# Optimization experiments

Measured on AMD Instinct MI355X. Metric: run time of the kernel, lower is better.

Reference implementation:

```python
import jax, jax.numpy as jnp
import numpy as np

B, N, E = 128, 196, 2048   # batch, num_features (14x14), encoder_dim
D, A = 512, 512            # decoder_dim, attention_dim


def setup_inputs() -> dict:
    key = jax.random.key(0)
    ks = jax.random.split(key, 8)
    s_e = 1.0 / np.sqrt(E)
    s_d = 1.0 / np.sqrt(D)
    s_a = 1.0 / np.sqrt(A)
    return {
        "encoder_out": jax.random.normal(ks[0], (B, N, E), dtype=jnp.float32),
        "decoder_hidden": jax.random.normal(ks[1], (B, D), dtype=jnp.float32),
        "We": jax.random.uniform(ks[2], (E, A), jnp.float32, -s_e, s_e),
        "be": jax.random.uniform(ks[3], (A,), jnp.float32, -s_e, s_e),
        "Wd": jax.random.uniform(ks[4], (D, A), jnp.float32, -s_d, s_d),
        "bd": jax.random.uniform(ks[5], (A,), jnp.float32, -s_d, s_d),
        "Wf": jax.random.uniform(ks[6], (A, 1), jnp.float32, -s_a, s_a),
        "bf": jax.random.uniform(ks[7], (1,), jnp.float32, -s_a, s_a),
    }


def reference(encoder_out, decoder_hidden, We, be, Wd, bd, Wf, bf):
    # att1: [B,N,A] projection of encoder features
    att1 = jnp.einsum('bne,ea->bna', encoder_out, We) + be
    # att2: [B,A] projection of decoder state, broadcast over N
    att2 = decoder_hidden @ Wd + bd
    att = jnp.tanh(att1 + att2[:, None, :])          # [B,N,A]
    scores = jnp.einsum('bna,ao->bno', att, Wf) + bf  # [B,N,1]
    alpha = jax.nn.softmax(scores, axis=1)            # softmax over num_features
    context = jnp.sum(encoder_out * alpha, axis=1)    # [B,E]
    return (context, alpha)
```

## Files before the change

### kernel.cpp

```cpp
#include <hip/hip_runtime.h>
#include <hip/hip_bf16.h>
#include <stdint.h>

#define B_   128
#define N_   196
#define E_   2048
#define D_   512
#define A_   512
#define MTOT (B_ * N_)

typedef short  short8  __attribute__((ext_vector_type(8)));
typedef float  floatx4 __attribute__((ext_vector_type(4)));

__device__ __forceinline__ unsigned short f2bf(float f) {
    union { float f; uint32_t u; } v; v.f = f;
    uint32_t r = v.u + 0x7FFFu + ((v.u >> 16) & 1u);
    return (unsigned short)(r >> 16);
}

__device__ __forceinline__ uint32_t pkbf(float a, float b) {
    uint32_t ua = __float_as_uint(a) + 0x8000u;
    uint32_t ub = __float_as_uint(b) + 0x8000u;
    return __builtin_amdgcn_perm(ub, ua, 0x07060302u);
}

__global__ void transcvt_k(const float* __restrict__ We, unsigned short* __restrict__ WeT) {
    __shared__ float tile[32][33];
    const int e0 = blockIdx.x * 32, a0 = blockIdx.y * 32;
    const int t = threadIdx.x, tc = t & 31, tr = t >> 5;
#pragma unroll
    for (int i = 0; i < 4; ++i) {
        int r = tr + i * 8;
        tile[r][tc] = We[(size_t)(e0 + r) * A_ + a0 + tc];
    }
    __syncthreads();
#pragma unroll
    for (int i = 0; i < 4; ++i) {
        int r = tr + i * 8;
        WeT[(size_t)(a0 + r) * E_ + e0 + tc] = f2bf(tile[tc][r]);
    }
}

__launch_bounds__(512)
__global__ void att2_k(const float* __restrict__ dh, const float* __restrict__ Wd,
                       const float* __restrict__ bd, const float* __restrict__ be,
                       float* __restrict__ att2p) {
    const int b = blockIdx.x, t = threadIdx.x;
    __shared__ float sdh[D_];
    sdh[t] = dh[b * D_ + t];
    __syncthreads();
    float acc = 0.f;
#pragma unroll 8
    for (int d = 0; d < D_; ++d) acc += sdh[d] * Wd[(size_t)d * A_ + t];
    att2p[(size_t)b * A_ + t] = acc + bd[t] + be[t];
}

__launch_bounds__(256, 4)
__global__ void score_gemm(const float* __restrict__ enc,
                           const unsigned short* __restrict__ WeT,
                           const float* __restrict__ att2p,
                           const float* __restrict__ Wf,
                           float* __restrict__ scoresP) {
    __shared__ __align__(16) char sMem[2 * 16384];
    __shared__ float sPart[2][128];

    const int t   = threadIdx.x;
    const int w   = t >> 6;
    const int l   = t & 63;
    const int l15 = l & 15;
    const int q4  = l >> 4;
    const int wr  = w >> 1, wc = w & 1;

    const int v     = (blockIdx.x & 7) * 98 + (blockIdx.x >> 3);
    const int strip = v >> 2, colb = v & 3;
    const int row0  = strip * 128;
    const int c0    = colb * 128;

    floatx4 acc[4][4] = {};

    const int ar = t >> 1, ah = t & 1;
    const float* aSrcT = enc + (size_t)(row0 + ar) * E_ + ah * 16;
    const int aswz = (ar >> 1) & 3;
    const int aWr0 = ar * 64 + (((2 * ah)     ^ aswz) * 16);
    const int aWr1 = ar * 64 + (((2 * ah + 1) ^ aswz) * 16);

    const unsigned short* bSrc[2];
    int bDst[2];
#pragma unroll
    for (int j = 0; j < 2; ++j) {
        int s = w * 2 + j;
        int n = s * 16 + (l >> 2), p = l & 3;
        int q = p ^ ((n >> 1) & 3);
        bSrc[j] = WeT + (size_t)(c0 + n) * E_ + q * 8;
        bDst[j] = 8192 + s * 1024;
    }

    const int chR  = q4 ^ ((l15 >> 1) & 3);
    const int offA = (wr * 64 + l15) * 64 + chR * 16;
    const int offB = 8192 + (wc * 64 + l15) * 64 + chR * 16;

    {
        float4 a0 = *(const float4*)(aSrcT);
        float4 a1 = *(const float4*)(aSrcT + 4);
        float4 a2 = *(const float4*)(aSrcT + 8);
        float4 a3 = *(const float4*)(aSrcT + 12);
#pragma unroll
        for (int j = 0; j < 2; ++j)
            __builtin_amdgcn_global_load_lds(
                (const __attribute__((address_space(1))) uint32_t*)(bSrc[j]),
                (__attribute__((address_space(3))) uint32_t*)(sMem + bDst[j]), 16, 0, 0);
        uint4 w0, w1;
        w0.x = pkbf(a0.x, a0.y); w0.y = pkbf(a0.z, a0.w);
        w0.z = pkbf(a1.x, a1.y); w0.w = pkbf(a1.z, a1.w);
        w1.x = pkbf(a2.x, a2.y); w1.y = pkbf(a2.z, a2.w);
        w1.z = pkbf(a3.x, a3.y); w1.w = pkbf(a3.z, a3.w);
        *(uint4*)(sMem + aWr0) = w0;
        *(uint4*)(sMem + aWr1) = w1;
        __syncthreads();
    }

    int cur = 0;
#pragma unroll 2
    for (int kk = 0; kk < 64; ++kk) {
        const int nxt = cur ^ 16384;
        const int kn  = (kk + 1) & 63;

        float4 a0 = *(const float4*)(aSrcT + kn * 32);
        float4 a1 = *(const float4*)(aSrcT + kn * 32 + 4);
        float4 a2 = *(const float4*)(aSrcT + kn * 32 + 8);
        float4 a3 = *(const float4*)(aSrcT + kn * 32 + 12);
#pragma unroll
        for (int j = 0; j < 2; ++j)
            __builtin_amdgcn_global_load_lds(
                (const __attribute__((address_space(1))) uint32_t*)(bSrc[j] + kn * 32),
                (__attribute__((address_space(3))) uint32_t*)(sMem + nxt + bDst[j]), 16, 0, 0);

        short8 bfr[4];
#pragma unroll
        for (int ni = 0; ni < 4; ++ni)
            bfr[ni] = *(const short8*)(sMem + cur + offB + ni * 1024);
#pragma unroll
        for (int mi = 0; mi < 4; ++mi) {
            short8 a = *(const short8*)(sMem + cur + offA + mi * 1024);
            acc[mi][0] = __builtin_amdgcn_mfma_f32_16x16x32_bf16(a, bfr[0], acc[mi][0], 0, 0, 0);
            acc[mi][1] = __builtin_amdgcn_mfma_f32_16x16x32_bf16(a, bfr[1], acc[mi][1], 0, 0, 0);
            acc[mi][2] = __builtin_amdgcn_mfma_f32_16x16x32_bf16(a, bfr[2], acc[mi][2], 0, 0, 0);
            acc[mi][3] = __builtin_amdgcn_mfma_f32_16x16x32_bf16(a, bfr[3], acc[mi][3], 0, 0, 0);
        }

        uint4 w0, w1;
        w0.x = pkbf(a0.x, a0.y); w0.y = pkbf(a0.z, a0.w);
        w0.z = pkbf(a1.x, a1.y); w0.w = pkbf(a1.z, a1.w);
        w1.x = pkbf(a2.x, a2.y); w1.y = pkbf(a2.z, a2.w);
        w1.z = pkbf(a3.x, a3.y); w1.w = pkbf(a3.z, a3.w);
        *(uint4*)(sMem + nxt + aWr0) = w0;
        *(uint4*)(sMem + nxt + aWr1) = w1;
        __syncthreads();
        cur = nxt;
    }

    const int cbase = c0 + wc * 64;
    float wfv[4];
#pragma unroll
    for (int ni = 0; ni < 4; ++ni) wfv[ni] = Wf[cbase + ni * 16 + l15];

#pragma unroll
    for (int mi = 0; mi < 4; ++mi) {
#pragma unroll
        for (int r = 0; r < 4; ++r) {
            const int m    = wr * 64 + mi * 16 + q4 * 4 + r;
            const int grow = row0 + m;
            const int bb   = grow / N_;
            const float* a2p = att2p + (size_t)bb * A_ + cbase;
            float s = 0.f;
#pragma unroll
            for (int ni = 0; ni < 4; ++ni) {
                float vv = acc[mi][ni][r] + a2p[ni * 16 + l15];
                float e  = __expf(2.f * vv);
                float th = 1.f - 2.f / (e + 1.f);
                s += th * wfv[ni];
            }
            s += __shfl_xor(s, 1);
            s += __shfl_xor(s, 2);
            s += __shfl_xor(s, 4);
            s += __shfl_xor(s, 8);
            if (l15 == 0) sPart[wc][m] = s;
        }
    }
    __syncthreads();
    if (t < 128) {
        scoresP[(size_t)colb * MTOT + row0 + t] = sPart[0][t] + sPart[1][t];
    }
}

__launch_bounds__(256)
__global__ void ctx_sm_k(const float* __restrict__ enc, const float* __restrict__ sp,
                         float* __restrict__ alpha, float* __restrict__ ctx) {
    const int chunk = blockIdx.x, b = blockIdx.y;
    const int t = threadIdx.x, w = t >> 6, l = t & 63;
    const int tn = t >> 6, tc = t & 63;
    __shared__ float  sAl[N_];
    __shared__ float  red[8];
    __shared__ float4 sRed[256];

    float v = -3.0e38f;
    if (t < N_) {
        const int i = b * N_ + t;
        v = sp[i] + sp[MTOT + i] + sp[2 * MTOT + i] + sp[3 * MTOT + i];
    }
    float m = v;
#pragma unroll
    for (int off = 32; off >= 1; off >>= 1) m = fmaxf(m, __shfl_xor(m, off));
    if (l == 0) red[w] = m;
    __syncthreads();
    m = fmaxf(fmaxf(red[0], red[1]), fmaxf(red[2], red[3]));
    float e = 0.f;
    if (t < N_) e = __expf(v - m);
    float s = e;
#pragma unroll
    for (int off = 32; off >= 1; off >>= 1) s += __shfl_xor(s, off);
    if (l == 0) red[4 + w] = s;
    __syncthreads();
    s = red[4] + red[5] + red[6] + red[7];
    if (t < N_) {
        float al = e / s;
        sAl[t] = al;
        if (chunk == 0) alpha[b * N_ + t] = al;
    }
    __syncthreads();

    const float* base = enc + (size_t)b * N_ * E_ + chunk * 256 + tc * 4;
    float4 a = make_float4(0.f, 0.f, 0.f, 0.f);
#pragma unroll 7
    for (int n = tn; n < N_; n += 4) {
        float  al = sAl[n];
        float4 vv = *(const float4*)(base + (size_t)n * E_);
        a.x += al * vv.x; a.y += al * vv.y; a.z += al * vv.z; a.w += al * vv.w;
    }
    sRed[t] = a;
    __syncthreads();
    if (t < 64) {
        float4 r0 = sRed[t], r1 = sRed[t + 64], r2 = sRed[t + 128], r3 = sRed[t + 192];
        float4 o = make_float4(r0.x + r1.x + r2.x + r3.x, r0.y + r1.y + r2.y + r3.y,
                               r0.z + r1.z + r2.z + r3.z, r0.w + r1.w + r2.w + r3.w);
        *(float4*)(ctx + (size_t)b * E_ + chunk * 256 + t * 4) = o;
    }
}

extern "C" void kernel_launch(void* const* d_in, const int* in_sizes, int n_in,
                              void* d_out, int out_size, void* d_ws, size_t ws_size,
                              hipStream_t stream) {
    const float* enc = (const float*)d_in[0];
    const float* dh  = (const float*)d_in[1];
    const float* We  = (const float*)d_in[2];
    const float* be  = (const float*)d_in[3];
    const float* Wd  = (const float*)d_in[4];
    const float* bd  = (const float*)d_in[5];
    const float* Wf  = (const float*)d_in[6];

    float* out   = (float*)d_out;
    float* ctx   = out;
    float* alpha = out + B_ * E_;

    char* ws = (char*)d_ws;
    unsigned short* WeT  = (unsigned short*)ws;
    float* att2p         = (float*)(ws + (2u << 20));
    float* scoresP       = (float*)(ws + (2u << 20) + (256u << 10));

    transcvt_k <<<dim3(E_ / 32, A_ / 32), 256, 0, stream>>>(We, WeT);
    att2_k     <<<dim3(B_),              512, 0, stream>>>(dh, Wd, bd, be, att2p);
    score_gemm <<<dim3(4 * MTOT / 128),  256, 0, stream>>>(enc, WeT, att2p, Wf, scoresP);
    ctx_sm_k   <<<dim3(E_ / 256, B_),    256, 0, stream>>>(enc, scoresP, alpha, ctx);
}
```

Before: 441.2 us.

## Prefetch encoder tiles two K-steps ahead with explicit waitcnt and barriers

```diff
diff --git a/kernel.cpp b/kernel.cpp
--- a/kernel.cpp
+++ b/kernel.cpp
@@ -99,65 +99,77 @@
     const int offA = (wr * 64 + l15) * 64 + chR * 16;
     const int offB = 8192 + (wc * 64 + l15) * 64 + chR * 16;
 
+    float4 rA0, rA1, rA2, rA3, rB0, rB1, rB2, rB3;
+
     {
-        float4 a0 = *(const float4*)(aSrcT);
-        float4 a1 = *(const float4*)(aSrcT + 4);
-        float4 a2 = *(const float4*)(aSrcT + 8);
-        float4 a3 = *(const float4*)(aSrcT + 12);
 #pragma unroll
         for (int j = 0; j < 2; ++j)
             __builtin_amdgcn_global_load_lds(
                 (const __attribute__((address_space(1))) uint32_t*)(bSrc[j]),
                 (__attribute__((address_space(3))) uint32_t*)(sMem + bDst[j]), 16, 0, 0);
+        float4 p0 = *(const float4*)(aSrcT);
+        float4 p1 = *(const float4*)(aSrcT + 4);
+        float4 p2 = *(const float4*)(aSrcT + 8);
+        float4 p3 = *(const float4*)(aSrcT + 12);
+        rA0 = *(const float4*)(aSrcT + 32);
+        rA1 = *(const float4*)(aSrcT + 36);
+        rA2 = *(const float4*)(aSrcT + 40);
+        rA3 = *(const float4*)(aSrcT + 44);
         uint4 w0, w1;
-        w0.x = pkbf(a0.x, a0.y); w0.y = pkbf(a0.z, a0.w);
-        w0.z = pkbf(a1.x, a1.y); w0.w = pkbf(a1.z, a1.w);
-        w1.x = pkbf(a2.x, a2.y); w1.y = pkbf(a2.z, a2.w);
-        w1.z = pkbf(a3.x, a3.y); w1.w = pkbf(a3.z, a3.w);
+        w0.x = pkbf(p0.x, p0.y); w0.y = pkbf(p0.z, p0.w);
+        w0.z = pkbf(p1.x, p1.y); w0.w = pkbf(p1.z, p1.w);
+        w1.x = pkbf(p2.x, p2.y); w1.y = pkbf(p2.z, p2.w);
+        w1.z = pkbf(p3.x, p3.y); w1.w = pkbf(p3.z, p3.w);
         *(uint4*)(sMem + aWr0) = w0;
         *(uint4*)(sMem + aWr1) = w1;
         __syncthreads();
     }
 
-    int cur = 0;
-#pragma unroll 2
-    for (int kk = 0; kk < 64; ++kk) {
-        const int nxt = cur ^ 16384;
-        const int kn  = (kk + 1) & 63;
-
-        float4 a0 = *(const float4*)(aSrcT + kn * 32);
-        float4 a1 = *(const float4*)(aSrcT + kn * 32 + 4);
-        float4 a2 = *(const float4*)(aSrcT + kn * 32 + 8);
-        float4 a3 = *(const float4*)(aSrcT + kn * 32 + 12);
-#pragma unroll
-        for (int j = 0; j < 2; ++j)
-            __builtin_amdgcn_global_load_lds(
-                (const __attribute__((address_space(1))) uint32_t*)(bSrc[j] + kn * 32),
-                (__attribute__((address_space(3))) uint32_t*)(sMem + nxt + bDst[j]), 16, 0, 0);
-
-        short8 bfr[4];
-#pragma unroll
-        for (int ni = 0; ni < 4; ++ni)
-            bfr[ni] = *(const short8*)(sMem + cur + offB + ni * 1024);
-#pragma unroll
-        for (int mi = 0; mi < 4; ++mi) {
-            short8 a = *(const short8*)(sMem + cur + offA + mi * 1024);
-            acc[mi][0] = __builtin_amdgcn_mfma_f32_16x16x32_bf16(a, bfr[0], acc[mi][0], 0, 0, 0);
-            acc[mi][1] = __builtin_amdgcn_mfma_f32_16x16x32_bf16(a, bfr[1], acc[mi][1], 0, 0, 0);
-            acc[mi][2] = __builtin_amdgcn_mfma_f32_16x16x32_bf16(a, bfr[2], acc[mi][2], 0, 0, 0);
-            acc[mi][3] = __builtin_amdgcn_mfma_f32_16x16x32_bf16(a, bfr[3], acc[mi][3], 0, 0, 0);
-        }
-
-        uint4 w0, w1;
-        w0.x = pkbf(a0.x, a0.y); w0.y = pkbf(a0.z, a0.w);
-        w0.z = pkbf(a1.x, a1.y); w0.w = pkbf(a1.z, a1.w);
-        w1.x = pkbf(a2.x, a2.y); w1.y = pkbf(a2.z, a2.w);
-        w1.z = pkbf(a3.x, a3.y); w1.w = pkbf(a3.z, a3.w);
-        *(uint4*)(sMem + nxt + aWr0) = w0;
-        *(uint4*)(sMem + nxt + aWr1) = w1;
-        __syncthreads();
-        cur = nxt;
-    }
+#define KSTEP(CUROFF, NXTOFF, RO0, RO1, RO2, RO3, RN0, RN1, RN2, RN3, KK)        \
+    {                                                                             \
+        const int kn1 = ((KK) + 1) & 63;                                          \
+        const int kn2 = ((KK) + 2) & 63;                                          \
+        _Pragma("unroll")                                                         \
+        for (int j = 0; j < 2; ++j)                                               \
+            __builtin_amdgcn_global_load_lds(                                     \
+                (const __attribute__((address_space(1))) uint32_t*)(bSrc[j] + kn1 * 32), \
+                (__attribute__((address_space(3))) uint32_t*)(sMem + (NXTOFF) + bDst[j]), 16, 0, 0); \
+        __builtin_amdgcn_sched_barrier(0);                                        \
+        RN0 = *(const float4*)(aSrcT + kn2 * 32);                                 \
+        RN1 = *(const float4*)(aSrcT + kn2 * 32 + 4);                             \
+        RN2 = *(const float4*)(aSrcT + kn2 * 32 + 8);                             \
+        RN3 = *(const float4*)(aSrcT + kn2 * 32 + 12);                            \
+        __builtin_amdgcn_sched_barrier(0);                                        \
+        short8 bfr[4];                                                            \
+        _Pragma("unroll")                                                         \
+        for (int ni = 0; ni < 4; ++ni)                                            \
+            bfr[ni] = *(const short8*)(sMem + (CUROFF) + offB + ni * 1024);       \
+        _Pragma("unroll")                                                         \
+        for (int mi = 0; mi < 4; ++mi) {                                          \
+            short8 a = *(const short8*)(sMem + (CUROFF) + offA + mi * 1024);      \
+            acc[mi][0] = __builtin_amdgcn_mfma_f32_16x16x32_bf16(a, bfr[0], acc[mi][0], 0, 0, 0); \
+            acc[mi][1] = __builtin_amdgcn_mfma_f32_16x16x32_bf16(a, bfr[1], acc[mi][1], 0, 0, 0); \
+            acc[mi][2] = __builtin_amdgcn_mfma_f32_16x16x32_bf16(a, bfr[2], acc[mi][2], 0, 0, 0); \
+            acc[mi][3] = __builtin_amdgcn_mfma_f32_16x16x32_bf16(a, bfr[3], acc[mi][3], 0, 0, 0); \
+        }                                                                         \
+        {                                                                         \
+            uint4 w0, w1;                                                         \
+            w0.x = pkbf(RO0.x, RO0.y); w0.y = pkbf(RO0.z, RO0.w);                 \
+            w0.z = pkbf(RO1.x, RO1.y); w0.w = pkbf(RO1.z, RO1.w);                 \
+            w1.x = pkbf(RO2.x, RO2.y); w1.y = pkbf(RO2.z, RO2.w);                 \
+            w1.z = pkbf(RO3.x, RO3.y); w1.w = pkbf(RO3.z, RO3.w);                 \
+            *(uint4*)(sMem + (NXTOFF) + aWr0) = w0;                               \
+            *(uint4*)(sMem + (NXTOFF) + aWr1) = w1;                               \
+        }                                                                         \
+        asm volatile("s_waitcnt lgkmcnt(0) vmcnt(4)" ::: "memory");               \
+        __builtin_amdgcn_s_barrier();                                             \
+    }
+
+    for (int kk = 0; kk < 64; kk += 2) {
+        KSTEP(0,     16384, rA0, rA1, rA2, rA3, rB0, rB1, rB2, rB3, kk);
+        KSTEP(16384, 0,     rB0, rB1, rB2, rB3, rA0, rA1, rA2, rA3, kk + 1);
+    }
+#undef KSTEP
 
     const int cbase = c0 + wc * 64;
     float wfv[4];
```

Result: slower. 552.1 us (+25.1%).

## Stage fp32 encoder tile directly to LDS, convert to bf16 at fragment load

Applied to the files above, without the earlier changes.

```diff
diff --git a/kernel.cpp b/kernel.cpp
--- a/kernel.cpp
+++ b/kernel.cpp
@@ -61,7 +61,7 @@
                            const float* __restrict__ att2p,
                            const float* __restrict__ Wf,
                            float* __restrict__ scoresP) {
-    __shared__ __align__(16) char sMem[2 * 16384];
+    __shared__ __align__(16) char sMem[24576];
     __shared__ float sPart[2][128];
 
     const int t   = threadIdx.x;
@@ -78,11 +78,15 @@
 
     floatx4 acc[4][4] = {};
 
-    const int ar = t >> 1, ah = t & 1;
-    const float* aSrcT = enc + (size_t)(row0 + ar) * E_ + ah * 16;
-    const int aswz = (ar >> 1) & 3;
-    const int aWr0 = ar * 64 + (((2 * ah)     ^ aswz) * 16);
-    const int aWr1 = ar * 64 + (((2 * ah + 1) ^ aswz) * 16);
+    const float* aSrc[4];
+    int aDst[4];
+#pragma unroll
+    for (int j = 0; j < 4; ++j) {
+        int s = (w * 4 + j) * 64 + l;
+        int r = s >> 3, pc = s & 7;
+        aSrc[j] = enc + (size_t)(row0 + r) * E_ + ((pc ^ (r & 7)) * 4);
+        aDst[j] = (w * 4 + j) * 1024;
+    }
 
     const unsigned short* bSrc[2];
     int bDst[2];
@@ -92,71 +96,51 @@
         int n = s * 16 + (l >> 2), p = l & 3;
         int q = p ^ ((n >> 1) & 3);
         bSrc[j] = WeT + (size_t)(c0 + n) * E_ + q * 8;
-        bDst[j] = 8192 + s * 1024;
-    }
-
-    const int chR  = q4 ^ ((l15 >> 1) & 3);
-    const int offA = (wr * 64 + l15) * 64 + chR * 16;
-    const int offB = 8192 + (wc * 64 + l15) * 64 + chR * 16;
-
-    {
-        float4 a0 = *(const float4*)(aSrcT);
-        float4 a1 = *(const float4*)(aSrcT + 4);
-        float4 a2 = *(const float4*)(aSrcT + 8);
-        float4 a3 = *(const float4*)(aSrcT + 12);
+        bDst[j] = 16384 + s * 1024;
+    }
+
+    const int pLo    = (2 * q4) ^ (l15 & 7);
+    const int offAlo = (wr * 64 + l15) * 128 + pLo * 16;
+    const int offAhi = (wr * 64 + l15) * 128 + (pLo ^ 1) * 16;
+    const int chB    = q4 ^ ((l15 >> 1) & 3);
+    const int offB   = 16384 + (wc * 64 + l15) * 64 + chB * 16;
+
+#pragma unroll 2
+    for (int kk = 0; kk < 64; ++kk) {
+#pragma unroll
+        for (int j = 0; j < 4; ++j)
+            __builtin_amdgcn_global_load_lds(
+                (const __attribute__((address_space(1))) uint32_t*)(aSrc[j] + kk * 32),
+                (__attribute__((address_space(3))) uint32_t*)(sMem + aDst[j]), 16, 0, 0);
 #pragma unroll
         for (int j = 0; j < 2; ++j)
             __builtin_amdgcn_global_load_lds(
-                (const __attribute__((address_space(1))) uint32_t*)(bSrc[j]),
+                (const __attribute__((address_space(1))) uint32_t*)(bSrc[j] + kk * 32),
                 (__attribute__((address_space(3))) uint32_t*)(sMem + bDst[j]), 16, 0, 0);
-        uint4 w0, w1;
-        w0.x = pkbf(a0.x, a0.y); w0.y = pkbf(a0.z, a0.w);
-        w0.z = pkbf(a1.x, a1.y); w0.w = pkbf(a1.z, a1.w);
-        w1.x = pkbf(a2.x, a2.y); w1.y = pkbf(a2.z, a2.w);
-        w1.z = pkbf(a3.x, a3.y); w1.w = pkbf(a3.z, a3.w);
-        *(uint4*)(sMem + aWr0) = w0;
-        *(uint4*)(sMem + aWr1) = w1;
         __syncthreads();
-    }
-
-    int cur = 0;
-#pragma unroll 2
-    for (int kk = 0; kk < 64; ++kk) {
-        const int nxt = cur ^ 16384;
-        const int kn  = (kk + 1) & 63;
-
-        float4 a0 = *(const float4*)(aSrcT + kn * 32);
-        float4 a1 = *(const float4*)(aSrcT + kn * 32 + 4);
-        float4 a2 = *(const float4*)(aSrcT + kn * 32 + 8);
-        float4 a3 = *(const float4*)(aSrcT + kn * 32 + 12);
-#pragma unroll
-        for (int j = 0; j < 2; ++j)
-            __builtin_amdgcn_global_load_lds(
-                (const __attribute__((address_space(1))) uint32_t*)(bSrc[j] + kn * 32),
-                (__attribute__((address_space(3))) uint32_t*)(sMem + nxt + bDst[j]), 16, 0, 0);
 
         short8 bfr[4];
+        union { uint32_t u[4]; short8 s; } af[4];
 #pragma unroll
         for (int ni = 0; ni < 4; ++ni)
-            bfr[ni] = *(const short8*)(sMem + cur + offB + ni * 1024);
+            bfr[ni] = *(const short8*)(sMem + offB + ni * 1024);
 #pragma unroll
         for (int mi = 0; mi < 4; ++mi) {
-            short8 a = *(const short8*)(sMem + cur + offA + mi * 1024);
-            acc[mi][0] = __builtin_amdgcn_mfma_f32_16x16x32_bf16(a, bfr[0], acc[mi][0], 0, 0, 0);
-            acc[mi][1] = __builtin_amdgcn_mfma_f32_16x16x32_bf16(a, bfr[1], acc[mi][1], 0, 0, 0);
-            acc[mi][2] = __builtin_amdgcn_mfma_f32_16x16x32_bf16(a, bfr[2], acc[mi][2], 0, 0, 0);
-            acc[mi][3] = __builtin_amdgcn_mfma_f32_16x16x32_bf16(a, bfr[3], acc[mi][3], 0, 0, 0);
+            float4 lo = *(const float4*)(sMem + offAlo + mi * 2048);
+            float4 hi = *(const float4*)(sMem + offAhi + mi * 2048);
+            af[mi].u[0] = pkbf(lo.x, lo.y);
+            af[mi].u[1] = pkbf(lo.z, lo.w);
+            af[mi].u[2] = pkbf(hi.x, hi.y);
+            af[mi].u[3] = pkbf(hi.z, hi.w);
         }
-
-        uint4 w0, w1;
-        w0.x = pkbf(a0.x, a0.y); w0.y = pkbf(a0.z, a0.w);
-        w0.z = pkbf(a1.x, a1.y); w0.w = pkbf(a1.z, a1.w);
-        w1.x = pkbf(a2.x, a2.y); w1.y = pkbf(a2.z, a2.w);
-        w1.z = pkbf(a3.x, a3.y); w1.w = pkbf(a3.z, a3.w);
-        *(uint4*)(sMem + nxt + aWr0) = w0;
-        *(uint4*)(sMem + nxt + aWr1) = w1;
+#pragma unroll
+        for (int mi = 0; mi < 4; ++mi) {
+            acc[mi][0] = __builtin_amdgcn_mfma_f32_16x16x32_bf16(af[mi].s, bfr[0], acc[mi][0], 0, 0, 0);
+            acc[mi][1] = __builtin_amdgcn_mfma_f32_16x16x32_bf16(af[mi].s, bfr[1], acc[mi][1], 0, 0, 0);
+            acc[mi][2] = __builtin_amdgcn_mfma_f32_16x16x32_bf16(af[mi].s, bfr[2], acc[mi][2], 0, 0, 0);
+            acc[mi][3] = __builtin_amdgcn_mfma_f32_16x16x32_bf16(af[mi].s, bfr[3], acc[mi][3], 0, 0, 0);
+        }
         __syncthreads();
-        cur = nxt;
     }
 
     const int cbase = c0 + wc * 64;
```

Result: faster. 430.3 us (-2.5%).
